# Optimization experiments

Hardware: AMD Instinct MI355X
Metric: run time of the kernel (lower is better)

Reference implementation:

```python
import jax, jax.numpy as jnp
import numpy as np

N, C, E, S = 16384, 128, 262144, 10
AVG_NUM_NEIGHBORS = 16.0
INV_SQRT3 = 1.0 / np.sqrt(3.0)


def setup_inputs() -> dict:
    key = jax.random.key(0)
    ks = jax.random.split(key, 15)
    return dict(
        node_specie=jax.random.randint(ks[0], (N,), 0, S),
        node_feats=jax.random.normal(ks[1], (N, C, 4), jnp.float32),   # irreps 0e+1o per channel
        edge_attrs=jax.random.normal(ks[2], (E, 4), jnp.float32),      # Y: 0e+1o
        edge_feats=jax.random.normal(ks[3], (E, 8), jnp.float32),      # radial scalars
        senders=jax.random.randint(ks[4], (E,), 0, N),
        receivers=jax.random.randint(ks[5], (E,), 0, N),
        W_sc0=jax.random.normal(ks[6], (S, C, C), jnp.float32),
        W_sc1=jax.random.normal(ks[7], (S, C, C), jnp.float32),
        W_pre0=jax.random.normal(ks[8], (C, C), jnp.float32),
        W_pre1=jax.random.normal(ks[9], (C, C), jnp.float32),
        W_mlp1=jax.random.normal(ks[10], (8, 64), jnp.float32),
        W_mlp2=jax.random.normal(ks[11], (64, 64), jnp.float32),
        W_mlp3=jax.random.normal(ks[12], (64, 4), jnp.float32),
        W_post0=jax.random.normal(ks[13], (C, 2, C), jnp.float32),
        W_post1=jax.random.normal(ks[14], (C, 2, C), jnp.float32),
    )


def reference(node_specie, node_feats, edge_attrs, edge_feats, senders, receivers,
              W_sc0, W_sc1, W_pre0, W_pre1, W_mlp1, W_mlp2, W_mlp3, W_post0, W_post1):
    inv_c = 1.0 / np.sqrt(C)
    s_in = node_feats[..., 0]      # [N,C] 0e
    v_in = node_feats[..., 1:4]    # [N,C,3] 1o

    # linear_sc: per-species equivariant linear (0e+1o -> hidden 0e+1o)
    sc_s = jnp.einsum('nc,ncd->nd', s_in, W_sc0[node_specie]) * inv_c
    sc_v = jnp.einsum('nci,ncd->ndi', v_in, W_sc1[node_specie]) * inv_c
    sc = jnp.concatenate([sc_s[..., None], sc_v], axis=-1)  # [N,C,4]

    # linear_premp: channel-mixing equivariant linear (same irreps)
    s = (s_in @ W_pre0) * inv_c                              # [N,C]
    v = jnp.einsum('nci,cd->ndi', v_in, W_pre1) * inv_c      # [N,C,3]

    # MessagePassingConvolution (channel axis kept instead of hk.vmap)
    se_s = s[senders]              # [E,C]
    se_v = v[senders]              # [E,C,3]
    a = edge_attrs[:, 1:4]         # drop 0e part of Y -> 1o
    dot = jnp.einsum('eci,ei->ec', se_v, a) * INV_SQRT3      # 1o x 1o -> 0e
    sva = se_s[..., None] * a[:, None, :]                    # 0e x 1o -> 1o

    # radial MLP -> one mixing scalar per irrep (num_irreps = 4), shared across channels
    h = jax.nn.silu((edge_feats @ W_mlp1) * (1.0 / np.sqrt(8.0)))
    h = jax.nn.silu((h @ W_mlp2) * 0.125)
    mix = (h @ W_mlp3) * 0.125                               # [E,4]

    # messages irreps 2x0e+2x1o: [s, dot | v, s*a], each block scaled by its mix scalar
    msg = jnp.concatenate([
        se_s[..., None] * mix[:, None, 0:1],
        dot[..., None] * mix[:, None, 1:2],
        se_v * mix[:, None, 2:3],
        sva * mix[:, None, 3:4],
    ], axis=-1)                                              # [E,C,8]

    agg = jnp.zeros((N, C, 8), msg.dtype).at[receivers].add(msg) / AVG_NUM_NEIGHBORS

    # linear_postmp: (2x0e+2x1o, C channels) -> (0e+1o, C channels)
    inv2c = 1.0 / np.sqrt(2 * C)
    o_s = jnp.einsum('ncm,cmd->nd', agg[..., :2], W_post0) * inv2c
    o_v = jnp.einsum('ncmi,cmd->ndi', agg[..., 2:].reshape(N, C, 2, 3), W_post1) * inv2c
    node_out = jnp.concatenate([o_s[..., None], o_v], axis=-1)  # [N,C,4]
    return node_out, sc
```

## Files before the change

kernel.cpp:

```cpp
#include <hip/hip_runtime.h>
#include <hip/hip_bf16.h>

#define N_NODES 16384
#define C_DIM   128
#define E_EDGES 262144
#define S_SPEC  10
#define PROWS   16544
#define PTILES  1034

__device__ __constant__ const float INV_C  = 0.08838834764831845f;
__device__ __constant__ const float INV_2C = 0.0625f;
#define F_INV_SQRT3 0.5773502691896258f
#define F_INV_SQRT8 0.35355339059327373f
#define F_INV_AVG   0.0625f

typedef __attribute__((ext_vector_type(8))) short bf16x8;
typedef __attribute__((ext_vector_type(4))) float f32x4;

__device__ __forceinline__ float silu(float x) {
    return x / (1.0f + __expf(-x));
}

__device__ __forceinline__ unsigned short f2bf(float x) {
    __hip_bfloat16 h = __float2bfloat16(x);
    return *reinterpret_cast<unsigned short*>(&h);
}

__device__ __forceinline__ unsigned int pack2bf(float lo, float hi) {
    return (unsigned int)f2bf(lo) | ((unsigned int)f2bf(hi) << 16);
}

__device__ __forceinline__ float bf2f(unsigned int u16) {
    return __uint_as_float(u16 << 16);
}

__global__ __launch_bounds__(256) void init_kernel(
    int* __restrict__ counts, int* __restrict__ scnt,
    int* __restrict__ prow_map, int* __restrict__ tile_spec)
{
    const int idx = blockIdx.x * 256 + threadIdx.x;
    if (idx < N_NODES) counts[idx] = 0;
    if (idx < S_SPEC)  scnt[idx] = 0;
    if (idx < PROWS)   prow_map[idx] = -1;
    if (idx < PTILES)  tile_spec[idx] = 0;
}

__global__ __launch_bounds__(256) void hist_kernel(
    const int* __restrict__ receivers, int* __restrict__ cnt,
    const int* __restrict__ specie, int* __restrict__ scnt)
{
    __shared__ int h[S_SPEC];
    const int t = threadIdx.x;
    const bool doSpec = blockIdx.x < (N_NODES / 256);
    if (doSpec) {
        if (t < S_SPEC) h[t] = 0;
        __syncthreads();
        atomicAdd(&h[specie[blockIdx.x * 256 + t]], 1);
    }
    const int e = blockIdx.x * 256 + t;
    atomicAdd(&cnt[receivers[e]], 1);
    if (doSpec) {
        __syncthreads();
        if (t < S_SPEC) atomicAdd(&scnt[t], h[t]);
    }
}

__global__ __launch_bounds__(256) void scan_kernel(
    const int* __restrict__ cnt, int* __restrict__ start,
    int* __restrict__ cursor,
    const int* __restrict__ scnt, int* __restrict__ poff,
    int* __restrict__ scur)
{
    __shared__ int sums[256];
    const int t = threadIdx.x;
    if (t == 0) {
        int pa = 0;
        for (int i = 0; i < S_SPEC; ++i) {
            poff[i] = pa;
            scur[i] = 0;
            pa += ((scnt[i] + 15) >> 4) << 4;
        }
    }
    int s = 0;
    for (int i = 0; i < 64; ++i) s += cnt[t * 64 + i];
    sums[t] = s;
    __syncthreads();
    if (t == 0) {
        int a = 0;
        for (int i = 0; i < 256; ++i) { int v = sums[i]; sums[i] = a; a += v; }
    }
    __syncthreads();
    int a = sums[t];
    for (int i = 0; i < 64; ++i) {
        int v = cnt[t * 64 + i];
        start[t * 64 + i] = a;
        cursor[t * 64 + i] = a;
        a += v;
    }
    if (t == 255) start[N_NODES] = a;
}

__global__ __launch_bounds__(256) void scatter_place_kernel(
    const int* __restrict__ receivers, int* __restrict__ cursor,
    int* __restrict__ perm,
    const int* __restrict__ specie, const int* __restrict__ poff,
    int* __restrict__ scur,
    int* __restrict__ prow_map, int* __restrict__ tile_spec)
{
    const int t = threadIdx.x;
    const int e = blockIdx.x * 256 + t;
    const int pos = atomicAdd(&cursor[receivers[e]], 1);
    perm[pos] = e;

    if (blockIdx.x < (N_NODES / 256)) {
        __shared__ int h[S_SPEC];
        __shared__ int bbase[S_SPEC];
        if (t < S_SPEC) h[t] = 0;
        __syncthreads();
        const int n = blockIdx.x * 256 + t;
        const int s = specie[n];
        const int lrank = atomicAdd(&h[s], 1);
        __syncthreads();
        if (t < S_SPEC && h[t] > 0) bbase[t] = atomicAdd(&scur[t], h[t]);
        __syncthreads();
        const int p = poff[s] + bbase[s] + lrank;
        prow_map[p] = n;
        tile_spec[p >> 4] = s;
    }
}

__global__ __launch_bounds__(256) void prep_kernel(
    const int* __restrict__ prow_map, const float* __restrict__ node_feats,
    ushort* __restrict__ As, ushort* __restrict__ Av0,
    ushort* __restrict__ Av1, ushort* __restrict__ Av2,
    const float* __restrict__ Wsc0, const float* __restrict__ Wsc1,
    ushort* __restrict__ Wsc0t, ushort* __restrict__ Wsc1t,
    const float* __restrict__ Wpre0, const float* __restrict__ Wpre1,
    ushort* __restrict__ Wpre0t, ushort* __restrict__ Wpre1t,
    const float* __restrict__ Wp0, const float* __restrict__ Wp1,
    ushort* __restrict__ Bt0, ushort* __restrict__ Bt1,
    const float* __restrict__ Wm1, const float* __restrict__ Wm2,
    const float* __restrict__ Wm3,
    ushort* __restrict__ W1t, ushort* __restrict__ W2t,
    ushort* __restrict__ W3t)
{
    const int idx = blockIdx.x * 256 + threadIdx.x;
    {
        const int p = idx >> 7, c = idx & 127;
        const int nid = prow_map[p];
        float4 f = {0.0f, 0.0f, 0.0f, 0.0f};
        if (nid >= 0) f = ((const float4*)node_feats)[nid * C_DIM + c];
        As [idx] = f2bf(f.x);
        Av0[idx] = f2bf(f.y);
        Av1[idx] = f2bf(f.z);
        Av2[idx] = f2bf(f.w);
    }
    if (idx < S_SPEC * 128 * 128) {
        const int s = idx >> 14, d = (idx >> 7) & 127, k = idx & 127;
        Wsc0t[idx] = f2bf(Wsc0[s * 16384 + k * 128 + d] * INV_C);
        Wsc1t[idx] = f2bf(Wsc1[s * 16384 + k * 128 + d] * INV_C);
    }
    if (idx < 16384) {
        const int d = idx >> 7, k = idx & 127;
        Wpre0t[idx] = f2bf(Wpre0[k * 128 + d] * INV_C);
        Wpre1t[idx] = f2bf(Wpre1[k * 128 + d] * INV_C);
    }
    if (idx < 32768) {
        const int k = idx >> 7, d = idx & 127;
        Bt0[d * 256 + k] = f2bf(Wp0[idx] * INV_2C);
        Bt1[d * 256 + k] = f2bf(Wp1[idx] * INV_2C);
    }
    if (idx < 4096) {
        if (idx < 2048) {
            const int hh = idx >> 5, k = idx & 31;
            W1t[idx] = (k < 8) ? f2bf(Wm1[k * 64 + hh] * F_INV_SQRT8) : (ushort)0;
        }
        {
            const int c = idx >> 6, k = idx & 63;
            W2t[idx] = f2bf(Wm2[k * 64 + c] * 0.125f);
        }
        if (idx < 1024) {
            const int m = idx >> 6, k = idx & 63;
            W3t[idx] = (m < 4) ? f2bf(Wm3[k * 4 + m] * 0.125f) : (ushort)0;
        }
    }
}

__global__ __launch_bounds__(512) void node_gemm_kernel(
    const int* __restrict__ prow_map,
    const int* __restrict__ tile_spec,
    const ushort* __restrict__ As,
    const ushort* __restrict__ Av0,
    const ushort* __restrict__ Av1,
    const ushort* __restrict__ Av2,
    const ushort* __restrict__ Wsc0t,
    const ushort* __restrict__ Wsc1t,
    const ushort* __restrict__ Wpre0t,
    const ushort* __restrict__ Wpre1t,
    float* __restrict__ out_sc,
    ushort4* __restrict__ sv_bf)
{
    const int l  = threadIdx.x & 63;
    const int w  = threadIdx.x >> 6;
    const int d0 = w * 16;
    const int lr = l & 15;
    const int lg = l >> 4;

    bf16x8 bp0[4], bp1[4];
#pragma unroll
    for (int ks = 0; ks < 4; ++ks) {
        bp0[ks] = *reinterpret_cast<const bf16x8*>(
            Wpre0t + (d0 + lr) * 128 + ks * 32 + lg * 8);
        bp1[ks] = *reinterpret_cast<const bf16x8*>(
            Wpre1t + (d0 + lr) * 128 + ks * 32 + lg * 8);
    }

    const int tile = blockIdx.x;
    const int sp   = tile_spec[tile];
    const int r0   = tile * 16;

    const ushort* as  = As  + (size_t)(r0 + lr) * 128 + lg * 8;
    const ushort* av0 = Av0 + (size_t)(r0 + lr) * 128 + lg * 8;
    const ushort* av1 = Av1 + (size_t)(r0 + lr) * 128 + lg * 8;
    const ushort* av2 = Av2 + (size_t)(r0 + lr) * 128 + lg * 8;
    const ushort* ws0 = Wsc0t + (size_t)sp * 16384 + (d0 + lr) * 128 + lg * 8;
    const ushort* ws1 = Wsc1t + (size_t)sp * 16384 + (d0 + lr) * 128 + lg * 8;

    const f32x4 zero = {0.0f, 0.0f, 0.0f, 0.0f};
    f32x4 aS0 = zero, aS1 = zero, aS2 = zero, aS3 = zero;
    f32x4 aP0 = zero, aP1 = zero, aP2 = zero, aP3 = zero;

#pragma unroll
    for (int ks = 0; ks < 4; ++ks) {
        const bf16x8 a_s  = *reinterpret_cast<const bf16x8*>(as  + ks * 32);
        const bf16x8 a_v0 = *reinterpret_cast<const bf16x8*>(av0 + ks * 32);
        const bf16x8 a_v1 = *reinterpret_cast<const bf16x8*>(av1 + ks * 32);
        const bf16x8 a_v2 = *reinterpret_cast<const bf16x8*>(av2 + ks * 32);
        const bf16x8 bs0  = *reinterpret_cast<const bf16x8*>(ws0 + ks * 32);
        const bf16x8 bs1  = *reinterpret_cast<const bf16x8*>(ws1 + ks * 32);
        aS0 = __builtin_amdgcn_mfma_f32_16x16x32_bf16(a_s,  bs0, aS0, 0, 0, 0);
        aS1 = __builtin_amdgcn_mfma_f32_16x16x32_bf16(a_v0, bs1, aS1, 0, 0, 0);
        aS2 = __builtin_amdgcn_mfma_f32_16x16x32_bf16(a_v1, bs1, aS2, 0, 0, 0);
        aS3 = __builtin_amdgcn_mfma_f32_16x16x32_bf16(a_v2, bs1, aS3, 0, 0, 0);
        aP0 = __builtin_amdgcn_mfma_f32_16x16x32_bf16(a_s,  bp0[ks], aP0, 0, 0, 0);
        aP1 = __builtin_amdgcn_mfma_f32_16x16x32_bf16(a_v0, bp1[ks], aP1, 0, 0, 0);
        aP2 = __builtin_amdgcn_mfma_f32_16x16x32_bf16(a_v1, bp1[ks], aP2, 0, 0, 0);
        aP3 = __builtin_amdgcn_mfma_f32_16x16x32_bf16(a_v2, bp1[ks], aP3, 0, 0, 0);
    }

#pragma unroll
    for (int r = 0; r < 4; ++r) {
        const int row = r0 + lg * 4 + r;
        const int nid = prow_map[row];
        if (nid >= 0) {
            float4 o = {aS0[r], aS1[r], aS2[r], aS3[r]};
            ((float4*)out_sc)[(size_t)nid * C_DIM + (d0 + lr)] = o;
            ushort4 pv = {f2bf(aP0[r]), f2bf(aP1[r]), f2bf(aP2[r]), f2bf(aP3[r])};
            sv_bf[(size_t)nid * C_DIM + (d0 + lr)] = pv;
        }
    }
}

__global__ __launch_bounds__(256) void edge_mlp_mfma_kernel(
    const float* __restrict__ edge_feats,
    const float* __restrict__ edge_attrs,
    const ushort* __restrict__ W1t,
    const ushort* __restrict__ W2t,
    const ushort* __restrict__ W3t,
    float* __restrict__ coef)
{
    __shared__ ushort h_lds[4][16][72];

    const int w  = threadIdx.x >> 6;
    const int l  = threadIdx.x & 63;
    const int lr = l & 15;
    const int lg = l >> 4;

    bf16x8 a1[4];
#pragma unroll
    for (int mt = 0; mt < 4; ++mt)
        a1[mt] = *reinterpret_cast<const bf16x8*>(
            W1t + (mt * 16 + lr) * 32 + lg * 8);
    bf16x8 a2[4][2];
#pragma unroll
    for (int mt = 0; mt < 4; ++mt)
#pragma unroll
        for (int ks = 0; ks < 2; ++ks)
            a2[mt][ks] = *reinterpret_cast<const bf16x8*>(
                W2t + (mt * 16 + lr) * 64 + ks * 32 + lg * 8);
    bf16x8 a3[2];
#pragma unroll
    for (int ks = 0; ks < 2; ++ks)
        a3[ks] = *reinterpret_cast<const bf16x8*>(
            W3t + lr * 64 + ks * 32 + lg * 8);

    const int tile = blockIdx.x * 4 + w;
    const int e0   = tile * 16;
    const f32x4 zero = {0.0f, 0.0f, 0.0f, 0.0f};

    bf16x8 b1 = {0, 0, 0, 0, 0, 0, 0, 0};
    if (lg == 0) {
        const float4 q0 = *(const float4*)(edge_feats + (size_t)(e0 + lr) * 8);
        const float4 q1 = *(const float4*)(edge_feats + (size_t)(e0 + lr) * 8 + 4);
        b1[0] = (short)f2bf(q0.x); b1[1] = (short)f2bf(q0.y);
        b1[2] = (short)f2bf(q0.z); b1[3] = (short)f2bf(q0.w);
        b1[4] = (short)f2bf(q1.x); b1[5] = (short)f2bf(q1.y);
        b1[6] = (short)f2bf(q1.z); b1[7] = (short)f2bf(q1.w);
    }

    f32x4 d1[4];
#pragma unroll
    for (int mt = 0; mt < 4; ++mt)
        d1[mt] = __builtin_amdgcn_mfma_f32_16x16x32_bf16(a1[mt], b1, zero, 0, 0, 0);

#pragma unroll
    for (int mt = 0; mt < 4; ++mt) {
        uint2 p;
        p.x = pack2bf(silu(d1[mt][0]), silu(d1[mt][1]));
        p.y = pack2bf(silu(d1[mt][2]), silu(d1[mt][3]));
        *reinterpret_cast<uint2*>(&h_lds[w][lr][mt * 16 + lg * 4]) = p;
    }
    __syncthreads();

    bf16x8 b2[2];
#pragma unroll
    for (int ks = 0; ks < 2; ++ks)
        b2[ks] = *reinterpret_cast<const bf16x8*>(
            &h_lds[w][lr][ks * 32 + lg * 8]);

    f32x4 d2[4];
#pragma unroll
    for (int mt = 0; mt < 4; ++mt) {
        d2[mt] = __builtin_amdgcn_mfma_f32_16x16x32_bf16(a2[mt][0], b2[0], zero, 0, 0, 0);
        d2[mt] = __builtin_amdgcn_mfma_f32_16x16x32_bf16(a2[mt][1], b2[1], d2[mt], 0, 0, 0);
    }

#pragma unroll
    for (int mt = 0; mt < 4; ++mt) {
        uint2 p;
        p.x = pack2bf(silu(d2[mt][0]), silu(d2[mt][1]));
        p.y = pack2bf(silu(d2[mt][2]), silu(d2[mt][3]));
        *reinterpret_cast<uint2*>(&h_lds[w][lr][mt * 16 + lg * 4]) = p;
    }
    __syncthreads();

    bf16x8 b3[2];
#pragma unroll
    for (int ks = 0; ks < 2; ++ks)
        b3[ks] = *reinterpret_cast<const bf16x8*>(
            &h_lds[w][lr][ks * 32 + lg * 8]);

    f32x4 d3;
    d3 = __builtin_amdgcn_mfma_f32_16x16x32_bf16(a3[0], b3[0], zero, 0, 0, 0);
    d3 = __builtin_amdgcn_mfma_f32_16x16x32_bf16(a3[1], b3[1], d3, 0, 0, 0);

    if (lg == 0) {
        const int e = e0 + lr;
        const float4 a = *(const float4*)(edge_attrs + (size_t)e * 4);
        const float mx0 = d3[0], mx1 = d3[1], mx2 = d3[2], mx3 = d3[3];
        float4 c0 = {mx0, mx1 * a.y * F_INV_SQRT3,
                     mx1 * a.z * F_INV_SQRT3, mx1 * a.w * F_INV_SQRT3};
        float4 c1 = {mx2, mx3 * a.y, mx3 * a.z, mx3 * a.w};
        ((float4*)coef)[e * 2 + 0] = c0;
        ((float4*)coef)[e * 2 + 1] = c1;
    }
}

__global__ __launch_bounds__(256) void agg_kernel(
    const int* __restrict__ start,
    const int* __restrict__ perm,
    const int* __restrict__ senders,
    const float* __restrict__ coef,
    const uint4* __restrict__ sv16,
    unsigned int* __restrict__ A_s,
    unsigned int* __restrict__ A_v)
{
    const int n    = blockIdx.x * 4 + (threadIdx.x >> 6);
    const int lane = threadIdx.x & 63;

    const int beg = start[n];
    const int end = start[n + 1];
    const float4* coef4 = (const float4*)coef;

    float acc0[8] = {};
    float acc1[8] = {};

    int e_nx = 0, s_nx = 0;
    if (beg < end) {
        e_nx = __builtin_amdgcn_readfirstlane(perm[beg]);
        s_nx = __builtin_amdgcn_readfirstlane(senders[e_nx]);
    }

    for (int idx = beg; idx < end; ++idx) {
        const int e   = e_nx;
        const int snd = s_nx;
        if (idx + 1 < end) {
            e_nx = __builtin_amdgcn_readfirstlane(perm[idx + 1]);
            s_nx = __builtin_amdgcn_readfirstlane(senders[e_nx]);
        }
        const float4 k0 = coef4[(size_t)e * 2 + 0];
        const float4 k1 = coef4[(size_t)e * 2 + 1];
        const uint4  q  = sv16[(size_t)snd * 64 + lane];

        const float x0 = bf2f(q.x & 0xffff), y0 = bf2f(q.x >> 16);
        const float z0 = bf2f(q.y & 0xffff), w0 = bf2f(q.y >> 16);
        const float x1 = bf2f(q.z & 0xffff), y1 = bf2f(q.z >> 16);
        const float z1 = bf2f(q.w & 0xffff), w1 = bf2f(q.w >> 16);

        acc0[0] += x0 * k0.x;
        acc0[1] += y0 * k0.y + z0 * k0.z + w0 * k0.w;
        acc0[2] += y0 * k1.x;
        acc0[3] += z0 * k1.x;
        acc0[4] += w0 * k1.x;
        acc0[5] += x0 * k1.y;
        acc0[6] += x0 * k1.z;
        acc0[7] += x0 * k1.w;

        acc1[0] += x1 * k0.x;
        acc1[1] += y1 * k0.y + z1 * k0.z + w1 * k0.w;
        acc1[2] += y1 * k1.x;
        acc1[3] += z1 * k1.x;
        acc1[4] += w1 * k1.x;
        acc1[5] += x1 * k1.y;
        acc1[6] += x1 * k1.z;
        acc1[7] += x1 * k1.w;
    }

    uint2 vs;
    vs.x = pack2bf(acc0[0] * F_INV_AVG, acc0[1] * F_INV_AVG);
    vs.y = pack2bf(acc1[0] * F_INV_AVG, acc1[1] * F_INV_AVG);
    ((uint2*)A_s)[(size_t)n * 64 + lane] = vs;

    uint2 v0;
    v0.x = pack2bf(acc0[2] * F_INV_AVG, acc0[5] * F_INV_AVG);
    v0.y = pack2bf(acc1[2] * F_INV_AVG, acc1[5] * F_INV_AVG);
    ((uint2*)A_v)[((size_t)n * 3 + 0) * 64 + lane] = v0;

    uint2 v1;
    v1.x = pack2bf(acc0[3] * F_INV_AVG, acc0[6] * F_INV_AVG);
    v1.y = pack2bf(acc1[3] * F_INV_AVG, acc1[6] * F_INV_AVG);
    ((uint2*)A_v)[((size_t)n * 3 + 1) * 64 + lane] = v1;

    uint2 v2;
    v2.x = pack2bf(acc0[4] * F_INV_AVG, acc0[7] * F_INV_AVG);
    v2.y = pack2bf(acc1[4] * F_INV_AVG, acc1[7] * F_INV_AVG);
    ((uint2*)A_v)[((size_t)n * 3 + 2) * 64 + lane] = v2;
}

__global__ __launch_bounds__(512) void post_gemm_kernel(
    const ushort* __restrict__ A_s,
    const ushort* __restrict__ A_v,
    const ushort* __restrict__ Bt0,
    const ushort* __restrict__ Bt1,
    float* __restrict__ out)
{
    const int l  = threadIdx.x & 63;
    const int w  = threadIdx.x >> 6;
    const int d0 = w * 16;
    const int lr = l & 15;
    const int lg = l >> 4;

    const bool isS = blockIdx.x < 512;
    const ushort* A  = isS ? A_s : A_v;
    const ushort* Bt = isS ? Bt0 : Bt1;
    const int ntiles  = isS ? (N_NODES / 16) : (3 * N_NODES / 16);
    const int b0      = isS ? blockIdx.x : blockIdx.x - 512;
    const int gstride = isS ? 512 : 1024;

    bf16x8 bfrag[8];
#pragma unroll
    for (int ks = 0; ks < 8; ++ks) {
        bfrag[ks] = *reinterpret_cast<const bf16x8*>(
            Bt + (size_t)(d0 + lr) * 256 + ks * 32 + lg * 8);
    }

    for (int tile = b0; tile < ntiles; tile += gstride) {
        const int r0 = tile * 16;
        f32x4 acc = {0.0f, 0.0f, 0.0f, 0.0f};
        const ushort* ap = A + (size_t)(r0 + lr) * 256 + lg * 8;
#pragma unroll
        for (int ks = 0; ks < 8; ++ks) {
            bf16x8 a = *reinterpret_cast<const bf16x8*>(ap + ks * 32);
            acc = __builtin_amdgcn_mfma_f32_16x16x32_bf16(a, bfrag[ks], acc,
                                                          0, 0, 0);
        }
#pragma unroll
        for (int r = 0; r < 4; ++r) {
            const int row = r0 + lg * 4 + r;
            int n, comp;
            if (isS) { n = row; comp = 0; }
            else { n = row / 3; comp = 1 + (row - n * 3); }
            out[(size_t)n * 512 + (d0 + lr) * 4 + comp] = acc[r];
        }
    }
}

extern "C" void kernel_launch(void* const* d_in, const int* in_sizes, int n_in,
                              void* d_out, int out_size, void* d_ws, size_t ws_size,
                              hipStream_t stream)
{
    const int*   specie     = (const int*)d_in[0];
    const float* node_feats = (const float*)d_in[1];
    const float* edge_attrs = (const float*)d_in[2];
    const float* edge_feats = (const float*)d_in[3];
    const int*   senders    = (const int*)d_in[4];
    const int*   receivers  = (const int*)d_in[5];
    const float* Wsc0  = (const float*)d_in[6];
    const float* Wsc1  = (const float*)d_in[7];
    const float* Wpre0 = (const float*)d_in[8];
    const float* Wpre1 = (const float*)d_in[9];
    const float* Wm1   = (const float*)d_in[10];
    const float* Wm2   = (const float*)d_in[11];
    const float* Wm3   = (const float*)d_in[12];
    const float* Wp0   = (const float*)d_in[13];
    const float* Wp1   = (const float*)d_in[14];

    float* out_node = (float*)d_out;
    float* out_sc   = out_node + (size_t)N_NODES * C_DIM * 4;

    char* ws = (char*)d_ws;
    ushort4*      sv_bf = (ushort4*)ws;
    unsigned int* A_s   = (unsigned int*)(ws + (size_t)16 * 1024 * 1024);
    unsigned int* A_v   = A_s + (size_t)N_NODES * 128;
    float*        coef  = (float*)(A_v + (size_t)3 * N_NODES * 128);
    ushort*       Asin  = (ushort*)(coef + (size_t)E_EDGES * 8);
    ushort*       Av0in = Asin  + (size_t)PROWS * 128;
    ushort*       Av1in = Av0in + (size_t)PROWS * 128;
    ushort*       Av2in = Av1in + (size_t)PROWS * 128;
    ushort*       Bt0   = Av2in + (size_t)PROWS * 128;
    ushort*       Bt1   = Bt0 + 256 * 128;
    ushort*       Wsc0t = Bt1 + 256 * 128;
    ushort*       Wsc1t = Wsc0t + S_SPEC * 128 * 128;
    ushort*       Wpre0t = Wsc1t + S_SPEC * 128 * 128;
    ushort*       Wpre1t = Wpre0t + 128 * 128;
    ushort*       W1t   = Wpre1t + 128 * 128;
    ushort*       W2t   = W1t + 64 * 32;
    ushort*       W3t   = W2t + 64 * 64;
    int* counts    = (int*)(W3t + 16 * 64);
    int* start     = counts + N_NODES;
    int* cursor    = start + (N_NODES + 1);
    int* perm      = cursor + N_NODES;
    int* scnt      = perm + E_EDGES;
    int* poff      = scnt + S_SPEC;
    int* scur      = poff + S_SPEC;
    int* prow_map  = scur + S_SPEC;
    int* tile_spec = prow_map + PROWS;

    init_kernel<<<(PROWS + 255) / 256, 256, 0, stream>>>(
        counts, scnt, prow_map, tile_spec);

    hist_kernel<<<E_EDGES / 256, 256, 0, stream>>>(
        receivers, counts, specie, scnt);

    scan_kernel<<<1, 256, 0, stream>>>(counts, start, cursor, scnt, poff, scur);

    scatter_place_kernel<<<E_EDGES / 256, 256, 0, stream>>>(
        receivers, cursor, perm, specie, poff, scur, prow_map, tile_spec);

    prep_kernel<<<PROWS * 128 / 256, 256, 0, stream>>>(
        prow_map, node_feats, Asin, Av0in, Av1in, Av2in,
        Wsc0, Wsc1, Wsc0t, Wsc1t, Wpre0, Wpre1, Wpre0t, Wpre1t,
        Wp0, Wp1, Bt0, Bt1, Wm1, Wm2, Wm3, W1t, W2t, W3t);

    node_gemm_kernel<<<PTILES, 512, 0, stream>>>(
        prow_map, tile_spec, Asin, Av0in, Av1in, Av2in,
        Wsc0t, Wsc1t, Wpre0t, Wpre1t, out_sc, sv_bf);

    edge_mlp_mfma_kernel<<<E_EDGES / 64, 256, 0, stream>>>(
        edge_feats, edge_attrs, W1t, W2t, W3t, coef);

    agg_kernel<<<N_NODES / 4, 256, 0, stream>>>(
        start, perm, senders, coef, (const uint4*)sv_bf, A_s, A_v);

    post_gemm_kernel<<<1536, 512, 0, stream>>>(
        (const ushort*)A_s, (const ushort*)A_v, Bt0, Bt1, out_node);
}
```

Measured before the change: 236.2 us.

## Restructure aggregation to stage edge coefs in LDS per node group with channel slicing

The edge coefficients are stored as bf16 (16 bytes per edge instead of 32), which halves that write and read traffic. The aggregation kernel now assigns 32 nodes times 8 channel slices per block. It stages the sender index and decoded coefficients for a chunk of edges into LDS once per block, instead of doing a serial readfirstlane-chained perm/senders lookup per wavefront. Each 8-lane group handles one node's slice, which raises parallelism but yields narrower 128-byte sender-feature gathers, adds block barriers, and may cause load imbalance across nodes in a group. Rounding the coefficients to bf16 adds precision loss.

New measurement: 260.1 us. 1.1x slower.

```diff
diff --git a/kernel.cpp b/kernel.cpp
--- a/kernel.cpp
+++ b/kernel.cpp
@@ -5,6 +5,9 @@
 #define C_DIM   128
 #define E_EDGES 262144
 #define S_SPEC  10
+#define CHUNK   256
+#define GNODES  32
+#define NSLICE  8
 #define PROWS   16544
 #define PTILES  1034
 
@@ -267,7 +270,7 @@
     const ushort* __restrict__ W1t,
     const ushort* __restrict__ W2t,
     const ushort* __restrict__ W3t,
-    float* __restrict__ coef)
+    uint4* __restrict__ coefbf)
 {
     __shared__ ushort h_lds[4][16][72];
 
@@ -358,11 +361,12 @@
         const int e = e0 + lr;
         const float4 a = *(const float4*)(edge_attrs + (size_t)e * 4);
         const float mx0 = d3[0], mx1 = d3[1], mx2 = d3[2], mx3 = d3[3];
-        float4 c0 = {mx0, mx1 * a.y * F_INV_SQRT3,
-                     mx1 * a.z * F_INV_SQRT3, mx1 * a.w * F_INV_SQRT3};
-        float4 c1 = {mx2, mx3 * a.y, mx3 * a.z, mx3 * a.w};
-        ((float4*)coef)[e * 2 + 0] = c0;
-        ((float4*)coef)[e * 2 + 1] = c1;
+        uint4 cv;
+        cv.x = pack2bf(mx0,                      mx1 * a.y * F_INV_SQRT3);
+        cv.y = pack2bf(mx1 * a.z * F_INV_SQRT3,  mx1 * a.w * F_INV_SQRT3);
+        cv.z = pack2bf(mx2,                      mx3 * a.y);
+        cv.w = pack2bf(mx3 * a.z,                mx3 * a.w);
+        coefbf[e] = cv;
     }
 }
 
@@ -370,81 +374,97 @@
     const int* __restrict__ start,
     const int* __restrict__ perm,
     const int* __restrict__ senders,
-    const float* __restrict__ coef,
+    const uint4* __restrict__ coefbf,
     const uint4* __restrict__ sv16,
     unsigned int* __restrict__ A_s,
     unsigned int* __restrict__ A_v)
 {
-    const int n    = blockIdx.x * 4 + (threadIdx.x >> 6);
-    const int lane = threadIdx.x & 63;
+    __shared__ int   se_lds[CHUNK];
+    __shared__ float sc_lds[CHUNK][8];
+
+    const int slice = blockIdx.x & (NSLICE - 1);
+    const int n0    = (blockIdx.x >> 3) * GNODES;
+    const int t     = threadIdx.x;
+    const int g     = t & 7;
+    const int ns    = t >> 3;
+    const int n     = n0 + ns;
 
     const int beg = start[n];
     const int end = start[n + 1];
-    const float4* coef4 = (const float4*)coef;
+    const int blk_beg = start[n0];
+    const int blk_end = start[n0 + GNODES];
 
     float acc0[8] = {};
     float acc1[8] = {};
 
-    int e_nx = 0, s_nx = 0;
-    if (beg < end) {
-        e_nx = __builtin_amdgcn_readfirstlane(perm[beg]);
-        s_nx = __builtin_amdgcn_readfirstlane(senders[e_nx]);
-    }
-
-    for (int idx = beg; idx < end; ++idx) {
-        const int e   = e_nx;
-        const int snd = s_nx;
-        if (idx + 1 < end) {
-            e_nx = __builtin_amdgcn_readfirstlane(perm[idx + 1]);
-            s_nx = __builtin_amdgcn_readfirstlane(senders[e_nx]);
-        }
-        const float4 k0 = coef4[(size_t)e * 2 + 0];
-        const float4 k1 = coef4[(size_t)e * 2 + 1];
-        const uint4  q  = sv16[(size_t)snd * 64 + lane];
-
-        const float x0 = bf2f(q.x & 0xffff), y0 = bf2f(q.x >> 16);
-        const float z0 = bf2f(q.y & 0xffff), w0 = bf2f(q.y >> 16);
-        const float x1 = bf2f(q.z & 0xffff), y1 = bf2f(q.z >> 16);
-        const float z1 = bf2f(q.w & 0xffff), w1 = bf2f(q.w >> 16);
-
-        acc0[0] += x0 * k0.x;
-        acc0[1] += y0 * k0.y + z0 * k0.z + w0 * k0.w;
-        acc0[2] += y0 * k1.x;
-        acc0[3] += z0 * k1.x;
-        acc0[4] += w0 * k1.x;
-        acc0[5] += x0 * k1.y;
-        acc0[6] += x0 * k1.z;
-        acc0[7] += x0 * k1.w;
-
-        acc1[0] += x1 * k0.x;
-        acc1[1] += y1 * k0.y + z1 * k0.z + w1 * k0.w;
-        acc1[2] += y1 * k1.x;
-        acc1[3] += z1 * k1.x;
-        acc1[4] += w1 * k1.x;
-        acc1[5] += x1 * k1.y;
-        acc1[6] += x1 * k1.z;
-        acc1[7] += x1 * k1.w;
-    }
-
+    for (int cb = blk_beg; cb < blk_end; cb += CHUNK) {
+        const int cn = min(CHUNK, blk_end - cb);
+        __syncthreads();
+        for (int j = t; j < cn; j += 256) {
+            const int e = perm[cb + j];
+            se_lds[j] = senders[e];
+            const uint4 cv = coefbf[e];
+            float* kf = sc_lds[j];
+            kf[0] = bf2f(cv.x & 0xffff); kf[1] = bf2f(cv.x >> 16);
+            kf[2] = bf2f(cv.y & 0xffff); kf[3] = bf2f(cv.y >> 16);
+            kf[4] = bf2f(cv.z & 0xffff); kf[5] = bf2f(cv.z >> 16);
+            kf[6] = bf2f(cv.w & 0xffff); kf[7] = bf2f(cv.w >> 16);
+        }
+        __syncthreads();
+
+        const int lo = max(beg, cb);
+        const int hi = min(end, cb + cn);
+        for (int idx = lo; idx < hi; ++idx) {
+            const int j = idx - cb;
+            const int snd = se_lds[j];
+            const float* kf = sc_lds[j];
+            const uint4 q = sv16[(size_t)snd * 64 + slice * 8 + g];
+
+            const float x0 = bf2f(q.x & 0xffff), y0 = bf2f(q.x >> 16);
+            const float z0 = bf2f(q.y & 0xffff), w0 = bf2f(q.y >> 16);
+            const float x1 = bf2f(q.z & 0xffff), y1 = bf2f(q.z >> 16);
+            const float z1 = bf2f(q.w & 0xffff), w1 = bf2f(q.w >> 16);
+
+            acc0[0] += x0 * kf[0];
+            acc0[1] += y0 * kf[1] + z0 * kf[2] + w0 * kf[3];
+            acc0[2] += y0 * kf[4];
+            acc0[3] += z0 * kf[4];
+            acc0[4] += w0 * kf[4];
+            acc0[5] += x0 * kf[5];
+            acc0[6] += x0 * kf[6];
+            acc0[7] += x0 * kf[7];
+
+            acc1[0] += x1 * kf[0];
+            acc1[1] += y1 * kf[1] + z1 * kf[2] + w1 * kf[3];
+            acc1[2] += y1 * kf[4];
+            acc1[3] += z1 * kf[4];
+            acc1[4] += w1 * kf[4];
+            acc1[5] += x1 * kf[5];
+            acc1[6] += x1 * kf[6];
+            acc1[7] += x1 * kf[7];
+        }
+    }
+
+    const int chp = slice * 8 + g;
     uint2 vs;
     vs.x = pack2bf(acc0[0] * F_INV_AVG, acc0[1] * F_INV_AVG);
     vs.y = pack2bf(acc1[0] * F_INV_AVG, acc1[1] * F_INV_AVG);
-    ((uint2*)A_s)[(size_t)n * 64 + lane] = vs;
+    ((uint2*)A_s)[(size_t)n * 64 + chp] = vs;
 
     uint2 v0;
     v0.x = pack2bf(acc0[2] * F_INV_AVG, acc0[5] * F_INV_AVG);
     v0.y = pack2bf(acc1[2] * F_INV_AVG, acc1[5] * F_INV_AVG);
-    ((uint2*)A_v)[((size_t)n * 3 + 0) * 64 + lane] = v0;
+    ((uint2*)A_v)[((size_t)n * 3 + 0) * 64 + chp] = v0;
 
     uint2 v1;
     v1.x = pack2bf(acc0[3] * F_INV_AVG, acc0[6] * F_INV_AVG);
     v1.y = pack2bf(acc1[3] * F_INV_AVG, acc1[6] * F_INV_AVG);
-    ((uint2*)A_v)[((size_t)n * 3 + 1) * 64 + lane] = v1;
+    ((uint2*)A_v)[((size_t)n * 3 + 1) * 64 + chp] = v1;
 
     uint2 v2;
     v2.x = pack2bf(acc0[4] * F_INV_AVG, acc0[7] * F_INV_AVG);
     v2.y = pack2bf(acc1[4] * F_INV_AVG, acc1[7] * F_INV_AVG);
-    ((uint2*)A_v)[((size_t)n * 3 + 2) * 64 + lane] = v2;
+    ((uint2*)A_v)[((size_t)n * 3 + 2) * 64 + chp] = v2;
 }
 
 __global__ __launch_bounds__(512) void post_gemm_kernel(
@@ -522,8 +542,8 @@
     ushort4*      sv_bf = (ushort4*)ws;
     unsigned int* A_s   = (unsigned int*)(ws + (size_t)16 * 1024 * 1024);
     unsigned int* A_v   = A_s + (size_t)N_NODES * 128;
-    float*        coef  = (float*)(A_v + (size_t)3 * N_NODES * 128);
-    ushort*       Asin  = (ushort*)(coef + (size_t)E_EDGES * 8);
+    uint4*        coefbf= (uint4*)(A_v + (size_t)3 * N_NODES * 128);
+    ushort*       Asin  = (ushort*)(coefbf + (size_t)E_EDGES);
     ushort*       Av0in = Asin  + (size_t)PROWS * 128;
     ushort*       Av1in = Av0in + (size_t)PROWS * 128;
     ushort*       Av2in = Av1in + (size_t)PROWS * 128;
@@ -567,10 +587,10 @@
         Wsc0t, Wsc1t, Wpre0t, Wpre1t, out_sc, sv_bf);
 
     edge_mlp_mfma_kernel<<<E_EDGES / 64, 256, 0, stream>>>(
-        edge_feats, edge_attrs, W1t, W2t, W3t, coef);
-
-    agg_kernel<<<N_NODES / 4, 256, 0, stream>>>(
-        start, perm, senders, coef, (const uint4*)sv_bf, A_s, A_v);
+        edge_feats, edge_attrs, W1t, W2t, W3t, coefbf);
+
+    agg_kernel<<<NSLICE * (N_NODES / GNODES), 256, 0, stream>>>(
+        start, perm, senders, coefbf, (const uint4*)sv_bf, A_s, A_v);
 
     post_gemm_kernel<<<1536, 512, 0, stream>>>(
         (const ushort*)A_s, (const ushort*)A_v, Bt0, Bt1, out_node);
```
